# Optimization experiments

Hardware: AMD Instinct MI355X
Metric: run time of the kernel (lower is better)

## Reference

```python
import jax, jax.numpy as jnp
import numpy as np

N_NODES = 100000
N_PART = 5000
N_EDGES = 1000000
D_NODE = 128
D_PART = 128
D_ATT = 20


def setup_inputs() -> dict:
    key = jax.random.key(0)
    ks = jax.random.split(key, 20)
    inp = {
        "nodes_hidden": jax.random.normal(ks[0], (N_NODES, D_NODE), jnp.float32),
        "particles_hidden": jax.random.normal(ks[1], (N_PART, D_PART), jnp.float32),
        "global_rep": jax.random.normal(ks[2], (N_PART, D_NODE), jnp.float32),
        "src": jax.random.randint(ks[3], (N_EDGES,), 0, N_NODES, jnp.int32),
        "dst": jax.random.randint(ks[4], (N_EDGES,), 0, N_PART, jnp.int32),
        "key_W": jax.random.normal(ks[5], (D_NODE, D_ATT), jnp.float32) * 0.05,
        "key_b": jnp.zeros((D_ATT,), jnp.float32),
        "val_W": jax.random.normal(ks[6], (D_NODE, D_PART), jnp.float32) * 0.05,
        "val_b": jnp.zeros((D_PART,), jnp.float32),
        "q_W": jax.random.normal(ks[7], (D_PART + D_NODE, D_ATT), jnp.float32) * 0.05,
        "q_b": jnp.zeros((D_ATT,), jnp.float32),
        "W_ih": jax.random.normal(ks[8], (3 * D_PART, D_PART), jnp.float32) * 0.05,
        "W_hh": jax.random.normal(ks[9], (3 * D_PART, D_PART), jnp.float32) * 0.05,
        "b_ih": jnp.zeros((3 * D_PART,), jnp.float32),
        "b_hh": jnp.zeros((3 * D_PART,), jnp.float32),
        "ln_g": jnp.ones((D_PART,), jnp.float32),
        "ln_b": jnp.zeros((D_PART,), jnp.float32),
        "mlp_W1": jax.random.normal(ks[10], (D_PART, 64), jnp.float32) * 0.05,
        "mlp_b1": jnp.zeros((64,), jnp.float32),
        "mlp_W2": jax.random.normal(ks[11], (64, D_PART), jnp.float32) * 0.05,
        "mlp_b2": jnp.zeros((D_PART,), jnp.float32),
    }
    return inp


def reference(nodes_hidden, particles_hidden, global_rep, src, dst,
              key_W, key_b, val_W, val_b, q_W, q_b,
              W_ih, W_hh, b_ih, b_hh, ln_g, ln_b,
              mlp_W1, mlp_b1, mlp_W2, mlp_b2):
    norm = jnp.float32(1.0) / jnp.sqrt(jnp.float32(D_ATT))
    keys = nodes_hidden @ key_W + key_b          # [N, 20]
    vals = nodes_hidden @ val_W + val_b          # [N, P]
    q_in = jnp.concatenate([particles_hidden, global_rep], axis=1)
    query = q_in @ q_W + q_b                     # [Np, 20]

    # per-edge raw attention (ReLU'd copy in edges.data is unused downstream)
    att = jnp.sum(keys[src] * query[dst], axis=1) * norm     # [E]
    msg = att[:, None] * vals[src]                            # [E, P]
    weighted_sum = jax.ops.segment_sum(msg, dst, num_segments=particles_hidden.shape[0])

    # GRUCell(input=weighted_sum, hidden=particles_hidden), torch semantics
    gi = weighted_sum @ W_ih.T + b_ih
    gh = particles_hidden @ W_hh.T + b_hh
    i_r, i_z, i_n = jnp.split(gi, 3, axis=1)
    h_r, h_z, h_n = jnp.split(gh, 3, axis=1)
    r = jax.nn.sigmoid(i_r + h_r)
    z = jax.nn.sigmoid(i_z + h_z)
    n = jnp.tanh(i_n + r * h_n)
    h_new = (1.0 - z) * n + z * particles_hidden

    # LayerNorm (eps=1e-5)
    mu = jnp.mean(h_new, axis=-1, keepdims=True)
    var = jnp.mean(jnp.square(h_new - mu), axis=-1, keepdims=True)
    ln = (h_new - mu) * jax.lax.rsqrt(var + 1e-5) * ln_g + ln_b

    mlp_out = jax.nn.relu(ln @ mlp_W1 + mlp_b1) @ mlp_W2 + mlp_b2
    return particles_hidden + mlp_out
```

## Files before the change

### kernel.cpp

```cpp
#include <hip/hip_runtime.h>
#include <math.h>

#define N_NODES 100000
#define N_PART  5000
#define N_EDGES 1000000
#define D_NODE  128
#define D_PART  128
#define D_ATT   20
#define NBLK    128
#define EPB     ((N_EDGES + NBLK - 1) / NBLK)
#define TPV6    8
#define QBLKS   (N_PART / TPV6)

__device__ __forceinline__ float sigmoid_(float x) { return 1.f / (1.f + __expf(-x)); }
__device__ __forceinline__ float tanh_(float x)    { return 1.f - 2.f / (__expf(2.f * x) + 1.f); }

__device__ __forceinline__ void gru_body(float4 acc[4],
    float4 w0, float4 w1, float4 w2, float4 w3,
    float4 x0, float4 x1, float4 x2, float4 x3)
{
    acc[0].x += x0.x * w0.x + x0.y * w1.x + x0.z * w2.x + x0.w * w3.x;
    acc[0].y += x0.x * w0.y + x0.y * w1.y + x0.z * w2.y + x0.w * w3.y;
    acc[0].z += x0.x * w0.z + x0.y * w1.z + x0.z * w2.z + x0.w * w3.z;
    acc[0].w += x0.x * w0.w + x0.y * w1.w + x0.z * w2.w + x0.w * w3.w;
    acc[1].x += x1.x * w0.x + x1.y * w1.x + x1.z * w2.x + x1.w * w3.x;
    acc[1].y += x1.x * w0.y + x1.y * w1.y + x1.z * w2.y + x1.w * w3.y;
    acc[1].z += x1.x * w0.z + x1.y * w1.z + x1.z * w2.z + x1.w * w3.z;
    acc[1].w += x1.x * w0.w + x1.y * w1.w + x1.z * w2.w + x1.w * w3.w;
    acc[2].x += x2.x * w0.x + x2.y * w1.x + x2.z * w2.x + x2.w * w3.x;
    acc[2].y += x2.x * w0.y + x2.y * w1.y + x2.z * w2.y + x2.w * w3.y;
    acc[2].z += x2.x * w0.z + x2.y * w1.z + x2.z * w2.z + x2.w * w3.z;
    acc[2].w += x2.x * w0.w + x2.y * w1.w + x2.z * w2.w + x2.w * w3.w;
    acc[3].x += x3.x * w0.x + x3.y * w1.x + x3.z * w2.x + x3.w * w3.x;
    acc[3].y += x3.x * w0.y + x3.y * w1.y + x3.z * w2.y + x3.w * w3.y;
    acc[3].z += x3.x * w0.z + x3.y * w1.z + x3.z * w2.z + x3.w * w3.z;
    acc[3].w += x3.x * w0.w + x3.y * w1.w + x3.z * w2.w + x3.w * w3.w;
}

__global__ __launch_bounds__(256) void fused_front_kernel(
    const float* __restrict__ valW, const float* __restrict__ Wih,
    const float* __restrict__ Whh, float* __restrict__ Wbig,
    const float* __restrict__ valb, float* __restrict__ bvec,
    const int* __restrict__ dst, int* __restrict__ blockhist,
    const float* __restrict__ ph, const float* __restrict__ gr,
    const float* __restrict__ qW, const float* __restrict__ qb,
    const float* __restrict__ keyW, const float* __restrict__ keyb,
    float* __restrict__ qk, float* __restrict__ qoff)
{
    __shared__ float pool[5000];
    int blk = blockIdx.x;
    int t = threadIdx.x;

    if (blk < 512) {
        int idx = blk * 256 + t;
        int k = idx >> 9;
        int jn = idx & 511;
        int j = (jn & 3) * 128 + (jn >> 2);
        float v = 0.f;
        if (k < 128) {
            if (j < 384) {
                float acc = 0.f;
                #pragma unroll 8
                for (int m = 0; m < 128; m++)
                    acc += valW[k * 128 + m] * Wih[j * 128 + m];
                v = acc;
            }
        } else {
            int kp = k - 128;
            if (j < 256)       v = Whh[j * 128 + kp];
            else if (j >= 384) v = Whh[(j - 128) * 128 + kp];
        }
        Wbig[k * 512 + jn] = v;
    } else if (blk < 514) {
        int c = (blk - 512) * 256 + t;
        if (c < 384) {
            float acc = 0.f;
            #pragma unroll 8
            for (int m = 0; m < 128; m++) acc += valb[m] * Wih[c * 128 + m];
            bvec[c] = acc;
        }
    } else if (blk < 642) {
        int b = blk - 514;
        int* h = (int*)pool;
        for (int i = t; i < N_PART; i += 256) h[i] = 0;
        __syncthreads();
        int beg = b * EPB, end = min(beg + EPB, N_EDGES);
        for (int e = beg + t; e < end; e += 256)
            atomicAdd(&h[dst[e]], 1);
        __syncthreads();
        for (int i = t; i < N_PART; i += 256)
            blockhist[(size_t)b * N_PART + i] = h[i];
    } else {
        float (*s_in)[260] = (float (*)[260])pool;
        float (*s_q)[20]   = (float (*)[20])(pool + 2080);
        float (*s_kw)[21]  = (float (*)[21])(pool + 2240);
        float* s_kb = pool + 4928;
        float* s_qb = pool + 4948;

        int pbase = (blk - 642) * TPV6;

        for (int f = t; f < TPV6 * 64; f += 256) {
            int pl = f >> 6, r = f & 63;
            int c4 = r * 4;
            int p = pbase + pl;
            float4 v;
            if (c4 < 128) v = *(const float4*)(ph + (size_t)p * 128 + c4);
            else          v = *(const float4*)(gr + (size_t)p * 128 + (c4 - 128));
            *(float4*)&s_in[pl][c4] = v;
        }
        for (int f = t; f < 2560; f += 256) {
            int j = f / 20, a = f - j * 20;
            s_kw[j][a] = keyW[f];
        }
        if (t < 20) { s_kb[t] = keyb[t]; s_qb[t] = qb[t]; }
        __syncthreads();

        if (t < 160) {
            int pl = t / 20, a = t - (t / 20) * 20;
            float acc = s_qb[a];
            const float* qwp = qW + a;
            #pragma unroll 8
            for (int k = 0; k < 256; k++) acc += s_in[pl][k] * qwp[k * 20];
            s_q[pl][a] = acc;
        }
        __syncthreads();

        {
            int pl = t >> 5, j0 = (t & 31) * 4;
            float4 o;
            float acc0 = 0.f, acc1 = 0.f, acc2 = 0.f, acc3 = 0.f;
            #pragma unroll
            for (int a = 0; a < 20; a++) {
                float qv = s_q[pl][a];
                acc0 += qv * s_kw[j0][a];
                acc1 += qv * s_kw[j0 + 1][a];
                acc2 += qv * s_kw[j0 + 2][a];
                acc3 += qv * s_kw[j0 + 3][a];
            }
            o.x = acc0; o.y = acc1; o.z = acc2; o.w = acc3;
            *(float4*)(qk + (size_t)(pbase + pl) * 128 + j0) = o;

            if (t < TPV6) {
                float acc = 0.f;
                #pragma unroll
                for (int a = 0; a < 20; a++) acc += s_kb[a] * s_q[t][a];
                qoff[pbase + t] = acc;
            }
        }
    }
}

__global__ __launch_bounds__(256) void colscan_kernel(
    int* __restrict__ blockhist, int* __restrict__ totals)
{
    int i = blockIdx.x * 256 + threadIdx.x;
    if (i >= N_PART) return;
    int run = 0;
    for (int b = 0; b < NBLK; b++) {
        size_t idx = (size_t)b * N_PART + i;
        int v = blockhist[idx];
        blockhist[idx] = run;
        run += v;
    }
    totals[i] = run;
}

__global__ __launch_bounds__(256) void scan_kernel(
    const int* __restrict__ totals, int* __restrict__ offsets)
{
    __shared__ int ss[256];
    int t = threadIdx.x;
    const int CH = 20;
    int beg = t * CH;
    int end = min(beg + CH, N_PART);
    int lsum = 0;
    for (int i = beg; i < end; i++) lsum += totals[i];
    ss[t] = lsum;
    __syncthreads();
    for (int off = 1; off < 256; off <<= 1) {
        int v = (t >= off) ? ss[t - off] : 0;
        __syncthreads();
        ss[t] += v;
        __syncthreads();
    }
    int base = ss[t] - lsum;
    for (int i = beg; i < end; i++) {
        offsets[i] = base;
        base += totals[i];
    }
    if (t == 0) offsets[N_PART] = N_EDGES;
}

__global__ __launch_bounds__(256) void scatter_sorted_kernel(
    const int* __restrict__ src, const int* __restrict__ dst,
    const int* __restrict__ offsets, const int* __restrict__ blockhist,
    int* __restrict__ ssrc)
{
    __shared__ int cur[N_PART];
    int b = blockIdx.x;
    for (int i = threadIdx.x; i < N_PART; i += 256)
        cur[i] = offsets[i] + blockhist[(size_t)b * N_PART + i];
    __syncthreads();
    int beg = b * EPB, end = min(beg + EPB, N_EDGES);
    for (int e = beg + threadIdx.x; e < end; e += 256) {
        int d = dst[e];
        int pos = atomicAdd(&cur[d], 1);
        ssrc[pos] = src[e];
    }
}

__global__ __launch_bounds__(256) void edge_agg_kernel(
    const float* __restrict__ nodes, const float* __restrict__ qk,
    const float* __restrict__ qoff,
    const int* __restrict__ offsets, const int* __restrict__ ssrc,
    float* __restrict__ agg, float* __restrict__ att_sum)
{
    const float norm = 0.22360679774997896f;
    int p = blockIdx.x;
    int tid = threadIdx.x;
    int lane = tid & 63;
    int wave = tid >> 6;
    int half = lane >> 5;
    int colq = (lane & 31) * 4;

    const float4 q = *(const float4*)(qk + (size_t)p * 128 + colq);
    float qo = qoff[p];
    int beg = offsets[p], end = offsets[p + 1];
    int n = end - beg;
    int np = (n + 1) >> 1;
    int npfull = n >> 1;

    float4 a = {0.f, 0.f, 0.f, 0.f};
    float asum = 0.f;

    int pi = wave;
    for (; pi + 12 < npfull; pi += 16) {
        int e0 = beg + 2 * pi + half;
        int s0 = ssrc[e0];
        int s1 = ssrc[e0 + 8];
        int s2 = ssrc[e0 + 16];
        int s3 = ssrc[e0 + 24];
        float4 x0 = *(const float4*)(nodes + (size_t)s0 * 128 + colq);
        float4 x1 = *(const float4*)(nodes + (size_t)s1 * 128 + colq);
        float4 x2 = *(const float4*)(nodes + (size_t)s2 * 128 + colq);
        float4 x3 = *(const float4*)(nodes + (size_t)s3 * 128 + colq);
        float d0 = x0.x * q.x + x0.y * q.y + x0.z * q.z + x0.w * q.w;
        float d1 = x1.x * q.x + x1.y * q.y + x1.z * q.z + x1.w * q.w;
        float d2 = x2.x * q.x + x2.y * q.y + x2.z * q.z + x2.w * q.w;
        float d3 = x3.x * q.x + x3.y * q.y + x3.z * q.z + x3.w * q.w;
        #pragma unroll
        for (int off = 1; off <= 16; off <<= 1) {
            d0 += __shfl_xor(d0, off, 64);
            d1 += __shfl_xor(d1, off, 64);
            d2 += __shfl_xor(d2, off, 64);
            d3 += __shfl_xor(d3, off, 64);
        }
        float t0 = (d0 + qo) * norm;
        float t1 = (d1 + qo) * norm;
        float t2 = (d2 + qo) * norm;
        float t3 = (d3 + qo) * norm;
        a.x += t0 * x0.x + t1 * x1.x + t2 * x2.x + t3 * x3.x;
        a.y += t0 * x0.y + t1 * x1.y + t2 * x2.y + t3 * x3.y;
        a.z += t0 * x0.z + t1 * x1.z + t2 * x2.z + t3 * x3.z;
        a.w += t0 * x0.w + t1 * x1.w + t2 * x2.w + t3 * x3.w;
        asum += t0 + t1 + t2 + t3;
    }
    for (; pi < np; pi += 4) {
        int e0 = beg + 2 * pi;
        bool has1 = (e0 + 1 < end);
        int s0 = ssrc[e0];
        int s1 = has1 ? ssrc[e0 + 1] : s0;
        int s = half ? s1 : s0;
        float4 x = *(const float4*)(nodes + (size_t)s * 128 + colq);
        float d = x.x * q.x + x.y * q.y + x.z * q.z + x.w * q.w;
        #pragma unroll
        for (int off = 1; off <= 16; off <<= 1) d += __shfl_xor(d, off, 64);
        float att = (d + qo) * norm;
        if (half && !has1) att = 0.f;
        a.x += att * x.x; a.y += att * x.y; a.z += att * x.z; a.w += att * x.w;
        asum += att;
    }

    a.x += __shfl_xor(a.x, 32, 64);
    a.y += __shfl_xor(a.y, 32, 64);
    a.z += __shfl_xor(a.z, 32, 64);
    a.w += __shfl_xor(a.w, 32, 64);
    asum += __shfl_xor(asum, 32, 64);

    __shared__ float s_acc[4][128];
    __shared__ float s_as[4];
    if (lane < 32) {
        *(float4*)&s_acc[wave][colq] = a;
        if (lane == 0) s_as[wave] = asum;
    }
    __syncthreads();

    if (tid < 128) {
        float v = s_acc[0][tid] + s_acc[1][tid] + s_acc[2][tid] + s_acc[3][tid];
        agg[(size_t)p * 128 + tid] = v;
        if (tid == 0) att_sum[p] = s_as[0] + s_as[1] + s_as[2] + s_as[3];
    }
}

__global__ __launch_bounds__(256) void gru_fused_v6(
    const float* __restrict__ agg, const float* __restrict__ att_sum,
    const float* __restrict__ ph,
    const float* __restrict__ Wbig, const float* __restrict__ bvec,
    const float* __restrict__ bih, const float* __restrict__ bhh,
    const float* __restrict__ lng, const float* __restrict__ lnb,
    const float* __restrict__ W1, const float* __restrict__ b1,
    const float* __restrict__ W2, const float* __restrict__ b2,
    float* __restrict__ out)
{
    __shared__ float s_in[TPV6][256];
    __shared__ float s_ln[TPV6][128];
    __shared__ float s_hid[TPV6][64];

    int t = threadIdx.x;
    int pbase = blockIdx.x * TPV6;

    for (int f = t; f < TPV6 * 64; f += 256) {
        int pl = f >> 6, r = f & 63;
        int c4 = r * 4;
        int p = pbase + pl;
        float4 v;
        if (c4 < 128) v = *(const float4*)(agg + (size_t)p * 128 + c4);
        else          v = *(const float4*)(ph + (size_t)p * 128 + (c4 - 128));
        *(float4*)&s_in[pl][c4] = v;
    }

    int c  = t & 127;
    int j4 = c * 4;
    int pg = t >> 7;
    float4 cb, bv;
    cb.x = bih[c]       + bhh[c];        bv.x = bvec[c];
    cb.y = bih[128 + c] + bhh[128 + c];  bv.y = bvec[128 + c];
    cb.z = bih[256 + c];                 bv.z = bvec[256 + c];
    cb.w = bhh[256 + c];                 bv.w = 0.f;
    float4 acc[4];
    #pragma unroll
    for (int i = 0; i < 4; i++) {
        float as = att_sum[pbase + pg * 4 + i];
        acc[i].x = cb.x + as * bv.x;
        acc[i].y = cb.y + as * bv.y;
        acc[i].z = cb.z + as * bv.z;
        acc[i].w = cb.w + as * bv.w;
    }
    __syncthreads();

    const float* wp = Wbig + j4;
    float4 w0 = *(const float4*)(wp);
    float4 w1 = *(const float4*)(wp + 512);
    float4 w2 = *(const float4*)(wp + 1024);
    float4 w3 = *(const float4*)(wp + 1536);
    float4 x0 = *(const float4*)&s_in[pg * 4 + 0][0];
    float4 x1 = *(const float4*)&s_in[pg * 4 + 1][0];
    float4 x2 = *(const float4*)&s_in[pg * 4 + 2][0];
    float4 x3 = *(const float4*)&s_in[pg * 4 + 3][0];
    for (int k = 0; k < 256; k += 4) {
        float4 cw0 = w0, cw1 = w1, cw2 = w2, cw3 = w3;
        float4 cx0 = x0, cx1 = x1, cx2 = x2, cx3 = x3;
        if (k < 252) {
            const float* wn = wp + (size_t)(k + 4) * 512;
            w0 = *(const float4*)(wn);
            w1 = *(const float4*)(wn + 512);
            w2 = *(const float4*)(wn + 1024);
            w3 = *(const float4*)(wn + 1536);
            x0 = *(const float4*)&s_in[pg * 4 + 0][k + 4];
            x1 = *(const float4*)&s_in[pg * 4 + 1][k + 4];
            x2 = *(const float4*)&s_in[pg * 4 + 2][k + 4];
            x3 = *(const float4*)&s_in[pg * 4 + 3][k + 4];
        }
        gru_body(acc, cw0, cw1, cw2, cw3, cx0, cx1, cx2, cx3);
    }

    #pragma unroll
    for (int i = 0; i < 4; i++) {
        int pl = pg * 4 + i;
        float r = sigmoid_(acc[i].x);
        float z = sigmoid_(acc[i].y);
        float n = tanh_(acc[i].z + r * acc[i].w);
        float h = s_in[pl][128 + c];
        s_ln[pl][c] = (1.f - z) * n + z * h;
    }
    __syncthreads();

    {
        int wv = t >> 6, l = t & 63;
        for (int pl = wv; pl < TPV6; pl += 4) {
            float v0 = s_ln[pl][l * 2], v1 = s_ln[pl][l * 2 + 1];
            float sum = v0 + v1, sq = v0 * v0 + v1 * v1;
            #pragma unroll
            for (int off = 1; off <= 32; off <<= 1) {
                sum += __shfl_xor(sum, off, 64);
                sq  += __shfl_xor(sq, off, 64);
            }
            float mu = sum * (1.f / 128.f);
            float var = sq * (1.f / 128.f) - mu * mu;
            float rstd = rsqrtf(var + 1e-5f);
            s_ln[pl][l * 2]     = (v0 - mu) * rstd * lng[l * 2] + lnb[l * 2];
            s_ln[pl][l * 2 + 1] = (v1 - mu) * rstd * lng[l * 2 + 1] + lnb[l * 2 + 1];
        }
    }
    __syncthreads();

    for (int idx = t; idx < TPV6 * 64; idx += 256) {
        int pl = idx >> 6, u = idx & 63;
        float a0 = b1[u];
        #pragma unroll 4
        for (int k = 0; k < 128; k++) a0 += s_ln[pl][k] * W1[k * 64 + u];
        s_hid[pl][u] = fmaxf(a0, 0.f);
    }
    __syncthreads();

    for (int idx = t; idx < TPV6 * 32; idx += 256) {
        int pl = idx >> 5, qd = idx & 31;
        int c4 = qd * 4;
        float4 o = *(const float4*)(b2 + c4);
        #pragma unroll 4
        for (int u = 0; u < 64; u++) {
            float av = s_hid[pl][u];
            float4 w = *(const float4*)(W2 + u * 128 + c4);
            o.x += av * w.x; o.y += av * w.y; o.z += av * w.z; o.w += av * w.w;
        }
        float4 h4 = *(const float4*)&s_in[pl][128 + c4];
        float4 res;
        res.x = h4.x + o.x; res.y = h4.y + o.y;
        res.z = h4.z + o.z; res.w = h4.w + o.w;
        *(float4*)(out + (size_t)(pbase + pl) * 128 + c4) = res;
    }
}

extern "C" void kernel_launch(void* const* d_in, const int* in_sizes, int n_in,
                              void* d_out, int out_size, void* d_ws, size_t ws_size,
                              hipStream_t stream) {
    const float* nodes = (const float*)d_in[0];
    const float* ph    = (const float*)d_in[1];
    const float* gr    = (const float*)d_in[2];
    const int*   src   = (const int*)d_in[3];
    const int*   dst   = (const int*)d_in[4];
    const float* keyW  = (const float*)d_in[5];
    const float* keyb  = (const float*)d_in[6];
    const float* valW  = (const float*)d_in[7];
    const float* valb  = (const float*)d_in[8];
    const float* qW    = (const float*)d_in[9];
    const float* qb    = (const float*)d_in[10];
    const float* Wih   = (const float*)d_in[11];
    const float* Whh   = (const float*)d_in[12];
    const float* bih   = (const float*)d_in[13];
    const float* bhh   = (const float*)d_in[14];
    const float* lng   = (const float*)d_in[15];
    const float* lnb   = (const float*)d_in[16];
    const float* W1    = (const float*)d_in[17];
    const float* b1    = (const float*)d_in[18];
    const float* W2    = (const float*)d_in[19];
    const float* b2    = (const float*)d_in[20];
    float* out = (float*)d_out;

    float* ws_f      = (float*)d_ws;
    float* qk        = ws_f;
    float* qoff      = qk + 640000;
    float* agg       = qoff + 5008;
    float* att_sum   = agg + 640000;
    int*   totals    = (int*)(att_sum + 5008);
    int*   offsets   = totals + 5008;
    int*   blockhist = offsets + 5008;
    int*   ssrc      = blockhist + (size_t)NBLK * N_PART;
    float* Wbig      = (float*)(ssrc + 1000000);
    float* bvec      = Wbig + 131072;

    fused_front_kernel<<<512 + 2 + NBLK + QBLKS, 256, 0, stream>>>(
        valW, Wih, Whh, Wbig,
        valb, bvec,
        dst, blockhist,
        ph, gr, qW, qb, keyW, keyb, qk, qoff);

    colscan_kernel<<<(N_PART + 255) / 256, 256, 0, stream>>>(blockhist, totals);

    scan_kernel<<<1, 256, 0, stream>>>(totals, offsets);

    scatter_sorted_kernel<<<NBLK, 256, 0, stream>>>(src, dst, offsets, blockhist, ssrc);

    edge_agg_kernel<<<N_PART, 256, 0, stream>>>(nodes, qk, qoff, offsets, ssrc, agg, att_sum);

    gru_fused_v6<<<N_PART / TPV6, 256, 0, stream>>>(
        agg, att_sum, ph, Wbig, bvec, bih, bhh, lng, lnb, W1, b1, W2, b2, out);
}
```

Measured before the change: 280.6 us.

## Replace per-block histogram scan with global atomic counting sort and tiled weight GEMM

```diff
diff --git a/kernel.cpp b/kernel.cpp
--- a/kernel.cpp
+++ b/kernel.cpp
@@ -41,7 +41,7 @@
     const float* __restrict__ valW, const float* __restrict__ Wih,
     const float* __restrict__ Whh, float* __restrict__ Wbig,
     const float* __restrict__ valb, float* __restrict__ bvec,
-    const int* __restrict__ dst, int* __restrict__ blockhist,
+    const int* __restrict__ dst, int* __restrict__ totals,
     const float* __restrict__ ph, const float* __restrict__ gr,
     const float* __restrict__ qW, const float* __restrict__ qb,
     const float* __restrict__ keyW, const float* __restrict__ keyb,
@@ -51,36 +51,78 @@
     int blk = blockIdx.x;
     int t = threadIdx.x;
 
-    if (blk < 512) {
-        int idx = blk * 256 + t;
-        int k = idx >> 9;
-        int jn = idx & 511;
-        int j = (jn & 3) * 128 + (jn >> 2);
-        float v = 0.f;
-        if (k < 128) {
-            if (j < 384) {
-                float acc = 0.f;
-                #pragma unroll 8
-                for (int m = 0; m < 128; m++)
-                    acc += valW[k * 128 + m] * Wih[j * 128 + m];
-                v = acc;
+    if (blk < 12) {
+        float (*sA)[33] = (float (*)[33])pool;
+        float (*sB)[33] = (float (*)[33])(pool + 2112);
+        int bk = blk / 6, bj = blk - bk * 6;
+        int k0 = bk * 64, j0 = bj * 64;
+        int tk = t >> 4, tj = t & 15;
+        float acc[4][4];
+        #pragma unroll
+        for (int i = 0; i < 4; i++)
+            #pragma unroll
+            for (int j = 0; j < 4; j++) acc[i][j] = 0.f;
+
+        for (int mc = 0; mc < 128; mc += 32) {
+            #pragma unroll
+            for (int s = 0; s < 2; s++) {
+                int f = t + s * 256;
+                int r = f >> 3, c4 = (f & 7) * 4;
+                *(float4*)&sA[r][c4] = *(const float4*)(valW + (size_t)(k0 + r) * 128 + mc + c4);
+                *(float4*)&sB[r][c4] = *(const float4*)(Wih  + (size_t)(j0 + r) * 128 + mc + c4);
             }
-        } else {
+            __syncthreads();
+            #pragma unroll 8
+            for (int mm = 0; mm < 32; mm++) {
+                float a0 = sA[tk * 4 + 0][mm], a1 = sA[tk * 4 + 1][mm];
+                float a2 = sA[tk * 4 + 2][mm], a3 = sA[tk * 4 + 3][mm];
+                float b0 = sB[tj * 4 + 0][mm], b1 = sB[tj * 4 + 1][mm];
+                float b2 = sB[tj * 4 + 2][mm], b3 = sB[tj * 4 + 3][mm];
+                acc[0][0] += a0 * b0; acc[0][1] += a0 * b1; acc[0][2] += a0 * b2; acc[0][3] += a0 * b3;
+                acc[1][0] += a1 * b0; acc[1][1] += a1 * b1; acc[1][2] += a1 * b2; acc[1][3] += a1 * b3;
+                acc[2][0] += a2 * b0; acc[2][1] += a2 * b1; acc[2][2] += a2 * b2; acc[2][3] += a2 * b3;
+                acc[3][0] += a3 * b0; acc[3][1] += a3 * b1; acc[3][2] += a3 * b2; acc[3][3] += a3 * b3;
+            }
+            __syncthreads();
+        }
+        #pragma unroll
+        for (int i = 0; i < 4; i++) {
+            int k = k0 + tk * 4 + i;
+            #pragma unroll
+            for (int j = 0; j < 4; j++) {
+                int oj = j0 + tj * 4 + j;
+                Wbig[(size_t)k * 512 + (oj & 127) * 4 + (oj >> 7)] = acc[i][j];
+            }
+        }
+    } else if (blk < 14) {
+        for (int f = t; f < 8192; f += 256) {
+            int e = (blk - 12) * 8192 + f;
+            int k = e >> 7, c = e & 127;
+            Wbig[(size_t)k * 512 + c * 4 + 3] = 0.f;
+        }
+    } else if (blk < 142) {
+        #pragma unroll
+        for (int s = 0; s < 2; s++) {
+            int idx = 65536 + (blk - 14) * 512 + s * 256 + t;
+            int k = idx >> 9;
+            int jn = idx & 511;
+            int j = (jn & 3) * 128 + (jn >> 2);
             int kp = k - 128;
+            float v = 0.f;
             if (j < 256)       v = Whh[j * 128 + kp];
             else if (j >= 384) v = Whh[(j - 128) * 128 + kp];
-        }
-        Wbig[k * 512 + jn] = v;
-    } else if (blk < 514) {
-        int c = (blk - 512) * 256 + t;
+            Wbig[(size_t)k * 512 + jn] = v;
+        }
+    } else if (blk < 144) {
+        int c = (blk - 142) * 256 + t;
         if (c < 384) {
             float acc = 0.f;
             #pragma unroll 8
             for (int m = 0; m < 128; m++) acc += valb[m] * Wih[c * 128 + m];
             bvec[c] = acc;
         }
-    } else if (blk < 642) {
-        int b = blk - 514;
+    } else if (blk < 272) {
+        int b = blk - 144;
         int* h = (int*)pool;
         for (int i = t; i < N_PART; i += 256) h[i] = 0;
         __syncthreads();
@@ -89,7 +131,7 @@
             atomicAdd(&h[dst[e]], 1);
         __syncthreads();
         for (int i = t; i < N_PART; i += 256)
-            blockhist[(size_t)b * N_PART + i] = h[i];
+            if (h[i]) atomicAdd(&totals[i], h[i]);
     } else {
         float (*s_in)[260] = (float (*)[260])pool;
         float (*s_q)[20]   = (float (*)[20])(pool + 2080);
@@ -97,7 +139,7 @@
         float* s_kb = pool + 4928;
         float* s_qb = pool + 4948;
 
-        int pbase = (blk - 642) * TPV6;
+        int pbase = (blk - 272) * TPV6;
 
         for (int f = t; f < TPV6 * 64; f += 256) {
             int pl = f >> 6, r = f & 63;
@@ -127,7 +169,6 @@
 
         {
             int pl = t >> 5, j0 = (t & 31) * 4;
-            float4 o;
             float acc0 = 0.f, acc1 = 0.f, acc2 = 0.f, acc3 = 0.f;
             #pragma unroll
             for (int a = 0; a < 20; a++) {
@@ -137,7 +178,7 @@
                 acc2 += qv * s_kw[j0 + 2][a];
                 acc3 += qv * s_kw[j0 + 3][a];
             }
-            o.x = acc0; o.y = acc1; o.z = acc2; o.w = acc3;
+            float4 o; o.x = acc0; o.y = acc1; o.z = acc2; o.w = acc3;
             *(float4*)(qk + (size_t)(pbase + pl) * 128 + j0) = o;
 
             if (t < TPV6) {
@@ -150,23 +191,9 @@
     }
 }
 
-__global__ __launch_bounds__(256) void colscan_kernel(
-    int* __restrict__ blockhist, int* __restrict__ totals)
-{
-    int i = blockIdx.x * 256 + threadIdx.x;
-    if (i >= N_PART) return;
-    int run = 0;
-    for (int b = 0; b < NBLK; b++) {
-        size_t idx = (size_t)b * N_PART + i;
-        int v = blockhist[idx];
-        blockhist[idx] = run;
-        run += v;
-    }
-    totals[i] = run;
-}
-
 __global__ __launch_bounds__(256) void scan_kernel(
-    const int* __restrict__ totals, int* __restrict__ offsets)
+    const int* __restrict__ totals, int* __restrict__ offsets,
+    int* __restrict__ cur)
 {
     __shared__ int ss[256];
     int t = threadIdx.x;
@@ -186,23 +213,18 @@
     int base = ss[t] - lsum;
     for (int i = beg; i < end; i++) {
         offsets[i] = base;
+        cur[i] = base;
         base += totals[i];
     }
     if (t == 0) offsets[N_PART] = N_EDGES;
 }
 
-__global__ __launch_bounds__(256) void scatter_sorted_kernel(
+__global__ __launch_bounds__(256) void scatter_atomic_kernel(
     const int* __restrict__ src, const int* __restrict__ dst,
-    const int* __restrict__ offsets, const int* __restrict__ blockhist,
-    int* __restrict__ ssrc)
+    int* __restrict__ cur, int* __restrict__ ssrc)
 {
-    __shared__ int cur[N_PART];
-    int b = blockIdx.x;
-    for (int i = threadIdx.x; i < N_PART; i += 256)
-        cur[i] = offsets[i] + blockhist[(size_t)b * N_PART + i];
-    __syncthreads();
-    int beg = b * EPB, end = min(beg + EPB, N_EDGES);
-    for (int e = beg + threadIdx.x; e < end; e += 256) {
+    int stride = gridDim.x * 256;
+    for (int e = blockIdx.x * 256 + threadIdx.x; e < N_EDGES; e += stride) {
         int d = dst[e];
         int pos = atomicAdd(&cur[d], 1);
         ssrc[pos] = src[e];
@@ -464,22 +486,22 @@
     float* att_sum   = agg + 640000;
     int*   totals    = (int*)(att_sum + 5008);
     int*   offsets   = totals + 5008;
-    int*   blockhist = offsets + 5008;
-    int*   ssrc      = blockhist + (size_t)NBLK * N_PART;
+    int*   cur       = offsets + 5008;
+    int*   ssrc      = cur + 5008;
     float* Wbig      = (float*)(ssrc + 1000000);
     float* bvec      = Wbig + 131072;
 
-    fused_front_kernel<<<512 + 2 + NBLK + QBLKS, 256, 0, stream>>>(
+    hipMemsetAsync(totals, 0, N_PART * sizeof(int), stream);
+
+    fused_front_kernel<<<272 + QBLKS, 256, 0, stream>>>(
         valW, Wih, Whh, Wbig,
         valb, bvec,
-        dst, blockhist,
+        dst, totals,
         ph, gr, qW, qb, keyW, keyb, qk, qoff);
 
-    colscan_kernel<<<(N_PART + 255) / 256, 256, 0, stream>>>(blockhist, totals);
-
-    scan_kernel<<<1, 256, 0, stream>>>(totals, offsets);
-
-    scatter_sorted_kernel<<<NBLK, 256, 0, stream>>>(src, dst, offsets, blockhist, ssrc);
+    scan_kernel<<<1, 256, 0, stream>>>(totals, offsets, cur);
+
+    scatter_atomic_kernel<<<512, 256, 0, stream>>>(src, dst, cur, ssrc);
 
     edge_agg_kernel<<<N_PART, 256, 0, stream>>>(nodes, qk, qoff, offsets, ssrc, agg, att_sum);
 
```

New measurement: 316.1 us. 1.13x slower.
